# Optimization experiments

Hardware: AMD Instinct MI355X
Metric: run time of the kernel (lower is better)

## Reference

```python
import jax, jax.numpy as jnp
import numpy as np

B, T, C = 2, 2048, 2048
H, G, HS = 16, 4, 128          # n_head, n_query_groups, head_size
Q_PER_KV = H // G
SWS = 1024                      # sliding_window_size
ROPE_BASE = 10000.0


def apply_rope(x, cos, sin):
    # x: [..., T, d] with d == rope_n_elem (= head_size here); cos/sin: [T, d]
    d = x.shape[-1]
    x1, x2 = x[..., : d // 2], x[..., d // 2 :]
    rotated = jnp.concatenate((-x2, x1), axis=-1)
    return x * cos + rotated * sin


def setup_inputs() -> dict:
    key = jax.random.key(0)
    k1, k2, k3 = jax.random.split(key, 3)
    x = jax.random.normal(k1, (B, T, C), dtype=jnp.float32)
    # standard RoPE cache (litgpt-style)
    inv_freq = 1.0 / (ROPE_BASE ** (jnp.arange(0, HS, 2, dtype=jnp.float32) / HS))
    ang = jnp.outer(jnp.arange(T, dtype=jnp.float32), inv_freq)  # [T, HS/2]
    ang = jnp.concatenate((ang, ang), axis=-1)                    # [T, HS]
    cos, sin = jnp.cos(ang), jnp.sin(ang)
    W_attn = jax.random.normal(k2, ((H + 2 * G) * HS, C), dtype=jnp.float32) * 0.02
    W_proj = jax.random.normal(k3, (C, H * HS), dtype=jnp.float32) * 0.02
    return {"x": x, "cos": cos, "sin": sin, "W_attn": W_attn, "W_proj": W_proj}


def reference(x, cos, sin, W_attn, W_proj):
    # fused QKV projection: [B,T,(H+2G)*HS]
    qkv = x @ W_attn.T
    # split into groups: [B,T,G,q_per_kv+2,HS] -> [B,G,total,T,HS]
    qkv = qkv.reshape(B, T, G, Q_PER_KV + 2, HS).transpose(0, 2, 3, 1, 4)
    q = qkv[:, :, :Q_PER_KV]        # [B,G,q_per_kv,T,HS]
    k = qkv[:, :, Q_PER_KV]         # [B,G,T,HS]
    v = qkv[:, :, Q_PER_KV + 1]     # [B,G,T,HS]
    # inline RoPE (rotary_percentage=1.0 -> whole head rotated)
    q = apply_rope(q, cos, sin)
    k = apply_rope(k, cos, sin)
    # sliding-window causal mask: attend iff i-SWS < j <= i
    i = jnp.arange(T)[:, None]
    j = jnp.arange(T)[None, :]
    allowed = (j <= i) & (j > i - SWS)
    mask = jnp.where(allowed, 0.0, -jnp.inf).astype(x.dtype)  # [T,T]
    # grouped attention (k/v shared across q_per_kv heads per group, same math
    # as the torch expand+reshape)
    scale = 1.0 / np.sqrt(HS).astype(np.float32)
    scores = jnp.einsum("bgqtd,bgsd->bgqts", q, k) * scale + mask
    attn = jax.nn.softmax(scores, axis=-1)
    y = jnp.einsum("bgqts,bgsd->bgqtd", attn, v)  # [B,G,q_per_kv,T,HS]
    # [B,H,T,HS] -> [B,T,H*HS]
    y = y.reshape(B, H, T, HS).transpose(0, 2, 1, 3).reshape(B, T, H * HS)
    return y @ W_proj.T
```

## Files before the change

### kernel.cpp

```cpp
#include <hip/hip_runtime.h>
#include <hip/hip_bf16.h>
#include <cstdint>
#include <type_traits>

using bf16_t = __hip_bfloat16;
typedef __bf16 bf16x8 __attribute__((ext_vector_type(8)));
typedef float f32x4 __attribute__((ext_vector_type(4)));

typedef __attribute__((address_space(3))) uint32_t lds_u32_t;
typedef const __attribute__((address_space(1))) uint32_t glb_u32_t;

__global__ void cvt_f32_to_bf16(const float* __restrict__ in, bf16_t* __restrict__ out, int n8) {
  int stride = gridDim.x * blockDim.x;
  for (int i = blockIdx.x * blockDim.x + threadIdx.x; i < n8; i += stride) {
    const float4* p = reinterpret_cast<const float4*>(in) + (size_t)i * 2;
    float4 a = p[0];
    float4 b = p[1];
    bf16_t o[8];
    o[0] = __float2bfloat16(a.x); o[1] = __float2bfloat16(a.y);
    o[2] = __float2bfloat16(a.z); o[3] = __float2bfloat16(a.w);
    o[4] = __float2bfloat16(b.x); o[5] = __float2bfloat16(b.y);
    o[6] = __float2bfloat16(b.z); o[7] = __float2bfloat16(b.w);
    *reinterpret_cast<uint4*>(out + (size_t)i * 8) = *reinterpret_cast<const uint4*>(o);
  }
}

template <int BN, typename OutT>
__global__ __launch_bounds__(512, 2) void gemm256(const bf16_t* __restrict__ A,
                                                  const bf16_t* __restrict__ Bt,
                                                  OutT* __restrict__ C,
                                                  int M, int N, int K) {
  constexpr int JN = BN / 64;
  constexpr int JLO = (JN + 1) / 2;
  constexpr int BL = BN / 64;
  __shared__ __align__(16) bf16_t As[2 * 256 * 64];
  __shared__ __align__(16) bf16_t Bs[2 * BN * 64];
  const int tid = threadIdx.x;
  const int lane = tid & 63;
  const int w = tid >> 6;
  const int wm = w >> 2, wn = w & 3;
  const int lr = lane & 15, lc = lane >> 4;

  const int nwg = gridDim.x * gridDim.y;
  const int orig = blockIdx.y * gridDim.x + blockIdx.x;
  const int cpx = nwg >> 3;
  const int swz = (orig & 7) * cpx + (orig >> 3);
  const int bx = swz % gridDim.x, by = swz / gridDim.x;
  const int m0 = by * 256, n0 = bx * BN;

  const int srow = tid >> 3;
  const int scol = ((tid & 7) ^ (srow & 7)) * 8;
  const bf16_t* Asrc = A + (size_t)(m0 + srow) * K + scol;
  const bf16_t* Bsrc = Bt + (size_t)(n0 + srow) * K + scol;

  f32x4 acc[8][JN] = {};

  auto stageA = [&](int bufi, int kt) {
#pragma unroll
    for (int l = 0; l < 4; ++l)
      __builtin_amdgcn_global_load_lds(
          (glb_u32_t*)(Asrc + (size_t)kt * 64 + (size_t)l * 64 * K),
          (lds_u32_t*)(As + bufi * 16384 + l * 4096 + w * 512), 16, 0, 0);
  };
  auto stageB = [&](int bufi, int kt) {
#pragma unroll
    for (int l = 0; l < BL; ++l)
      __builtin_amdgcn_global_load_lds(
          (glb_u32_t*)(Bsrc + (size_t)kt * 64 + (size_t)l * 64 * K),
          (lds_u32_t*)(Bs + bufi * BN * 64 + l * 4096 + w * 512), 16, 0, 0);
  };

  const int nt = K >> 6;
  stageA(0, 0);
  stageB(0, 0);
  asm volatile("s_waitcnt vmcnt(0)" ::: "memory");
  __builtin_amdgcn_s_barrier();

  bf16x8 a[4][2], bb[JN][2];
  for (int t = 0; t < nt; ++t) {
    const int buf = t & 1;
    const char* Ab = (const char*)(As + buf * 16384);
    const char* Bb = (const char*)(Bs + buf * BN * 64);
    const bool st = (t + 1 < nt);

    auto rdA = [&](int i, int kk) {
      int R = wm * 128 + i * 16 + lr;
      return *reinterpret_cast<const bf16x8*>(
          Ab + R * 128 + ((kk * 64 + lc * 16) ^ ((R & 7) << 4)));
    };
    auto rdB = [&](int j, int kk) {
      int R = wn * (BN / 4) + j * 16 + lr;
      return *reinterpret_cast<const bf16x8*>(
          Bb + R * 128 + ((kk * 64 + lc * 16) ^ ((R & 7) << 4)));
    };

#pragma unroll
    for (int i = 0; i < 4; ++i) { a[i][0] = rdA(i, 0); a[i][1] = rdA(i, 1); }
#pragma unroll
    for (int j = 0; j < JLO; ++j) { bb[j][0] = rdB(j, 0); bb[j][1] = rdB(j, 1); }
    if (st) stageA(buf ^ 1, t + 1);
    asm volatile("" ::: "memory");
    __builtin_amdgcn_s_barrier();
    __builtin_amdgcn_s_setprio(1);
#pragma unroll
    for (int i = 0; i < 4; ++i)
#pragma unroll
      for (int j = 0; j < JLO; ++j) {
        acc[i][j] = __builtin_amdgcn_mfma_f32_16x16x32_bf16(a[i][0], bb[j][0], acc[i][j], 0, 0, 0);
        acc[i][j] = __builtin_amdgcn_mfma_f32_16x16x32_bf16(a[i][1], bb[j][1], acc[i][j], 0, 0, 0);
      }
    __builtin_amdgcn_s_setprio(0);
    asm volatile("" ::: "memory");
    __builtin_amdgcn_s_barrier();

#pragma unroll
    for (int j = JLO; j < JN; ++j) { bb[j][0] = rdB(j, 0); bb[j][1] = rdB(j, 1); }
    if (st) stageB(buf ^ 1, t + 1);
    asm volatile("" ::: "memory");
    __builtin_amdgcn_s_barrier();
    __builtin_amdgcn_s_setprio(1);
#pragma unroll
    for (int i = 0; i < 4; ++i)
#pragma unroll
      for (int j = JLO; j < JN; ++j) {
        acc[i][j] = __builtin_amdgcn_mfma_f32_16x16x32_bf16(a[i][0], bb[j][0], acc[i][j], 0, 0, 0);
        acc[i][j] = __builtin_amdgcn_mfma_f32_16x16x32_bf16(a[i][1], bb[j][1], acc[i][j], 0, 0, 0);
      }
    __builtin_amdgcn_s_setprio(0);
    asm volatile("" ::: "memory");
    __builtin_amdgcn_s_barrier();

#pragma unroll
    for (int i = 0; i < 4; ++i) { a[i][0] = rdA(i + 4, 0); a[i][1] = rdA(i + 4, 1); }
    asm volatile("" ::: "memory");
    __builtin_amdgcn_s_barrier();
    __builtin_amdgcn_s_setprio(1);
#pragma unroll
    for (int i = 0; i < 4; ++i)
#pragma unroll
      for (int j = JLO; j < JN; ++j) {
        acc[i + 4][j] = __builtin_amdgcn_mfma_f32_16x16x32_bf16(a[i][0], bb[j][0], acc[i + 4][j], 0, 0, 0);
        acc[i + 4][j] = __builtin_amdgcn_mfma_f32_16x16x32_bf16(a[i][1], bb[j][1], acc[i + 4][j], 0, 0, 0);
      }
    __builtin_amdgcn_s_setprio(0);
    asm volatile("" ::: "memory");
    __builtin_amdgcn_s_barrier();

    __builtin_amdgcn_s_setprio(1);
#pragma unroll
    for (int i = 0; i < 4; ++i)
#pragma unroll
      for (int j = 0; j < JLO; ++j) {
        acc[i + 4][j] = __builtin_amdgcn_mfma_f32_16x16x32_bf16(a[i][0], bb[j][0], acc[i + 4][j], 0, 0, 0);
        acc[i + 4][j] = __builtin_amdgcn_mfma_f32_16x16x32_bf16(a[i][1], bb[j][1], acc[i + 4][j], 0, 0, 0);
      }
    __builtin_amdgcn_s_setprio(0);

    asm volatile("s_waitcnt lgkmcnt(0)" ::: "memory");
    asm volatile("s_waitcnt vmcnt(0)" ::: "memory");
    __builtin_amdgcn_s_barrier();
  }

#pragma unroll
  for (int i = 0; i < 8; ++i)
#pragma unroll
    for (int j = 0; j < JN; ++j) {
      int row = m0 + wm * 128 + i * 16 + lc * 4;
      int col = n0 + wn * (BN / 4) + j * 16 + lr;
#pragma unroll
      for (int r = 0; r < 4; ++r) {
        float v = acc[i][j][r];
        if constexpr (std::is_same<OutT, float>::value)
          C[(size_t)(row + r) * N + col] = v;
        else
          C[(size_t)(row + r) * N + col] = __float2bfloat16(v);
      }
    }
}

__global__ __launch_bounds__(256) void rope_scatter(const bf16_t* __restrict__ qkv,
                                                    const float* __restrict__ cosp,
                                                    const float* __restrict__ sinp,
                                                    bf16_t* __restrict__ Q,
                                                    bf16_t* __restrict__ K,
                                                    bf16_t* __restrict__ V) {
  const int row = blockIdx.x;
  const int b = row >> 11, t = row & 2047;
  const bf16_t* src = qkv + (size_t)row * 3072;
  for (int n = threadIdx.x; n < 3072; n += 256) {
    int g = n / 768;
    int r = n - g * 768;
    int slot = r >> 7;
    int d = r & 127;
    if (slot == 5) {
      V[(((size_t)(b * 4 + g)) * 2048 + t) * 128 + d] = src[n];
    } else {
      float v = __bfloat162float(src[n]);
      float other = __bfloat162float(src[n ^ 64]);
      float c = cosp[t * 128 + d];
      float s = sinp[t * 128 + d];
      float rot = (d < 64) ? -other : other;
      float res = v * c + rot * s;
      if (slot < 4) {
        int h = g * 4 + slot;
        Q[(((size_t)(b * 16 + h)) * 2048 + t) * 128 + d] =
            __float2bfloat16(res * (0.08838834764831843f * 1.4426950408889634f));
      } else {
        K[(((size_t)(b * 4 + g)) * 2048 + t) * 128 + d] = __float2bfloat16(res);
      }
    }
  }
}

__global__ void transpose_v(const bf16_t* __restrict__ V, bf16_t* __restrict__ Vt) {
  __shared__ bf16_t tile[32][33];
  const int bg = blockIdx.z;
  const int t0 = blockIdx.x * 32;
  const int d0 = blockIdx.y * 32;
  const bf16_t* src = V + (size_t)bg * 2048 * 128;
  bf16_t* dst = Vt + (size_t)bg * 128 * 2048;
#pragma unroll
  for (int i = threadIdx.y; i < 32; i += 8)
    tile[i][threadIdx.x] = src[(size_t)(t0 + i) * 128 + d0 + threadIdx.x];
  __syncthreads();
#pragma unroll
  for (int i = threadIdx.y; i < 32; i += 8)
    dst[(size_t)(d0 + i) * 2048 + t0 + threadIdx.x] = tile[threadIdx.x][i];
}

#define VROW 40
__global__ __launch_bounds__(256) void attn_swa(const bf16_t* __restrict__ Q,
                                                const bf16_t* __restrict__ K,
                                                const bf16_t* __restrict__ Vt,
                                                bf16_t* __restrict__ Y) {
  __shared__ __align__(16) bf16_t Ks[2 * 32 * 128];
  __shared__ __align__(16) bf16_t Vs[2 * 128 * VROW];

  const int tid = threadIdx.x;
  const int lane = tid & 63;
  const int w = tid >> 6;
  const int lr = lane & 15, lc = lane >> 4;
  const int b = blockIdx.z, h = blockIdx.y;
  const int g = h >> 2;

  int nseg, sx0, sx1 = 0;
  if (blockIdx.x < 16) {
    nseg = 1;
    sx0 = blockIdx.x + 16;
  } else {
    nseg = 2;
    sx0 = blockIdx.x - 16;
    sx1 = 15 - sx0;
  }

  const bf16_t* Qp = Q + ((size_t)(b * 16 + h) * 2048) * 128;
  const bf16_t* Kp = K + ((size_t)(b * 4 + g) * 2048) * 128;
  const bf16_t* Vp = Vt + ((size_t)(b * 4 + g) * 128) * 2048;

  const int kmj = tid >> 4;
  const int kmc = ((tid & 15) ^ (kmj & 7)) * 8;
  const bf16_t* Ksrc = Kp + (size_t)kmj * 128 + kmc;
  const int vd = tid >> 2, vc = tid & 3;
  const bf16_t* Vsrc = Vp + (size_t)vd * 2048 + vc * 8;
  const int vdst = vd * VROW + (vc & 1) * 16 + (vc >> 1) * 4;

  auto loadK = [&](int j0, uint4& ka, uint4& kb) {
    const bf16_t* s = Ksrc + (size_t)j0 * 128;
    ka = *reinterpret_cast<const uint4*>(s);
    kb = *reinterpret_cast<const uint4*>(s + 16 * 128);
  };
  auto writeK = [&](int bufi, uint4 ka, uint4 kb) {
    *reinterpret_cast<uint4*>(Ks + bufi * 4096 + tid * 8) = ka;
    *reinterpret_cast<uint4*>(Ks + bufi * 4096 + 2048 + tid * 8) = kb;
  };
  auto loadV = [&](int j0, uint4& a, uint4& bqv) {
    a = *reinterpret_cast<const uint4*>(Vsrc + j0);
    bqv = *reinterpret_cast<const uint4*>(Vsrc + 64 * 2048 + j0);
  };
  auto writeV = [&](int bufi, uint4 a, uint4 bqv) {
    bf16_t* p = Vs + bufi * 128 * VROW + vdst;
    *reinterpret_cast<uint2*>(p) = make_uint2(a.x, a.y);
    *reinterpret_cast<uint2*>(p + 8) = make_uint2(a.z, a.w);
    bf16_t* p1 = p + 64 * VROW;
    *reinterpret_cast<uint2*>(p1) = make_uint2(bqv.x, bqv.y);
    *reinterpret_cast<uint2*>(p1 + 8) = make_uint2(bqv.z, bqv.w);
  };

  const int kxor = (lr & 7) << 4;

  for (int sidx = 0; sidx < nseg; ++sidx) {
    const int i0b = ((sidx == 0) ? sx0 : sx1) * 64;
    const int i0 = i0b + w * 16;
    const int qrow = i0 + lr;

    bf16x8 qf[4];
#pragma unroll
    for (int kc = 0; kc < 4; ++kc)
      qf[kc] = *reinterpret_cast<const bf16x8*>(&Qp[(size_t)qrow * 128 + kc * 32 + lc * 8]);

    f32x4 o[8] = {};
    float mrun = -1e30f, lrun = 0.f;

    int lo = i0b - 1023;
    if (lo < 0) lo = 0;
    const int jstart = lo & ~31;
    const int jlast = i0b + 32;

    {
      uint4 ka, kb, va, vb;
      loadK(jstart, ka, kb);
      loadV(jstart, va, vb);
      writeK(0, ka, kb);
      writeV(0, va, vb);
    }
    __syncthreads();

    int buf = 0;
    for (int j0 = jstart; j0 <= jlast; j0 += 32) {
      const int nxt = j0 + 32;
      uint4 ka, kb, va, vb;
      const bool do_stage = (nxt <= jlast);
      if (do_stage) {
        loadK(nxt, ka, kb);
        loadV(nxt, va, vb);
      }

      const bool active = (j0 <= i0 + 15) && (j0 + 31 > i0 - 1024);
      if (active) {
        const bf16_t* Kb = Ks + buf * 4096;
        const bf16_t* Vb = Vs + buf * 128 * VROW;
        f32x4 s0 = {}, s1 = {};
        __builtin_amdgcn_s_setprio(1);
#pragma unroll
        for (int kc = 0; kc < 4; ++kc) {
          int col = ((kc * 64 + lc * 16) ^ kxor) >> 1;
          bf16x8 kf0 = *reinterpret_cast<const bf16x8*>(Kb + lr * 128 + col);
          bf16x8 kf1 = *reinterpret_cast<const bf16x8*>(Kb + (16 + lr) * 128 + col);
          s0 = __builtin_amdgcn_mfma_f32_16x16x32_bf16(kf0, qf[kc], s0, 0, 0, 0);
          s1 = __builtin_amdgcn_mfma_f32_16x16x32_bf16(kf1, qf[kc], s1, 0, 0, 0);
        }
        __builtin_amdgcn_s_setprio(0);
        bf16x8 vvf[8];
#pragma unroll
        for (int f = 0; f < 8; ++f)
          vvf[f] = *reinterpret_cast<const bf16x8*>(Vb + (f * 16 + lr) * VROW + lc * 8);

        const bool full = (j0 + 31 <= i0) && (j0 >= i0 - 1008);
        if (!full) {
#pragma unroll
          for (int r = 0; r < 4; ++r) {
            int ja = j0 + lc * 4 + r;
            int jb = ja + 16;
            bool oka = (ja <= qrow) && (ja > qrow - 1024);
            bool okb = (jb <= qrow) && (jb > qrow - 1024);
            s0[r] = oka ? s0[r] : -1e30f;
            s1[r] = okb ? s1[r] : -1e30f;
          }
        }
        float rm = fmaxf(fmaxf(fmaxf(s0[0], s0[1]), fmaxf(s0[2], s0[3])),
                         fmaxf(fmaxf(s1[0], s1[1]), fmaxf(s1[2], s1[3])));

        if (!__all(rm <= mrun + 11.5f)) {
          rm = fmaxf(rm, __shfl_xor(rm, 16));
          rm = fmaxf(rm, __shfl_xor(rm, 32));
          float mnew = fmaxf(mrun, rm);
          float alpha = exp2f(mrun - mnew);
          mrun = mnew;
          lrun *= alpha;
#pragma unroll
          for (int f = 0; f < 8; ++f)
#pragma unroll
            for (int r = 0; r < 4; ++r) o[f][r] *= alpha;
        }

        float p0[4], p1[4], ps = 0.f;
#pragma unroll
        for (int r = 0; r < 4; ++r) {
          p0[r] = exp2f(s0[r] - mrun);
          p1[r] = exp2f(s1[r] - mrun);
          ps += p0[r] + p1[r];
        }
        lrun += ps;

        bf16_t pb[8];
#pragma unroll
        for (int r = 0; r < 4; ++r) {
          pb[r] = __float2bfloat16(p0[r]);
          pb[r + 4] = __float2bfloat16(p1[r]);
        }
        bf16x8 pfrag = *reinterpret_cast<bf16x8*>(pb);

        __builtin_amdgcn_s_setprio(1);
#pragma unroll
        for (int f = 0; f < 8; ++f)
          o[f] = __builtin_amdgcn_mfma_f32_16x16x32_bf16(vvf[f], pfrag, o[f], 0, 0, 0);
        __builtin_amdgcn_s_setprio(0);
      }

      if (do_stage) {
        writeK(buf ^ 1, ka, kb);
        writeV(buf ^ 1, va, vb);
      }
      __syncthreads();
      buf ^= 1;
    }

    float lt = lrun;
    lt += __shfl_xor(lt, 16);
    lt += __shfl_xor(lt, 32);
    float inv = 1.f / lt;
#pragma unroll
    for (int f = 0; f < 8; ++f) {
      bf16_t ob[4];
#pragma unroll
      for (int r = 0; r < 4; ++r) ob[r] = __float2bfloat16(o[f][r] * inv);
      *reinterpret_cast<uint2*>(
          &Y[((size_t)(b * 2048 + qrow)) * 2048 + h * 128 + f * 16 + lc * 4]) =
          *reinterpret_cast<uint2*>(ob);
    }
  }
}

extern "C" void kernel_launch(void* const* d_in, const int* in_sizes, int n_in,
                              void* d_out, int out_size, void* d_ws, size_t ws_size,
                              hipStream_t stream) {
  const float* x = (const float*)d_in[0];
  const float* cosp = (const float*)d_in[1];
  const float* sinp = (const float*)d_in[2];
  const float* Wa = (const float*)d_in[3];
  const float* Wp = (const float*)d_in[4];
  float* out = (float*)d_out;

  bf16_t* ws = (bf16_t*)d_ws;
  bf16_t* xb = ws;
  bf16_t* wab = ws + 8388608;
  bf16_t* wpb = ws + 14680064;
  bf16_t* qkv = ws + 18874368;
  bf16_t* Q = xb;
  bf16_t* Kr = wab;
  bf16_t* V = wab + 2097152;
  bf16_t* Y = qkv;
  bf16_t* Vt = qkv + 8388608;

  cvt_f32_to_bf16<<<4096, 256, 0, stream>>>(x, xb, 1048576);
  cvt_f32_to_bf16<<<3072, 256, 0, stream>>>(Wa, wab, 786432);
  cvt_f32_to_bf16<<<2048, 256, 0, stream>>>(Wp, wpb, 524288);

  gemm256<192, bf16_t><<<dim3(16, 16), 512, 0, stream>>>(xb, wab, qkv, 4096, 3072, 2048);

  rope_scatter<<<4096, 256, 0, stream>>>(qkv, cosp, sinp, Q, Kr, V);

  transpose_v<<<dim3(64, 4, 8), dim3(32, 8), 0, stream>>>(V, Vt);

  attn_swa<<<dim3(24, 16, 2), 256, 0, stream>>>(Q, Kr, Vt, Y);

  gemm256<128, float><<<dim3(16, 16), 512, 0, stream>>>(Y, wpb, out, 4096, 2048, 2048);
}
```

Measured before the change: 226.1 us.

## Restructure GEMM main loop into one MFMA phase with partial vmcnt waits

Replaces the four-phase ping-pong loop in gemm256 with a single phase per K-tile. Each tile now does one load of all A and B fragments followed by one MFMA block. Synchronisation relies on partial s_waitcnt vmcnt counts, so the next tile's async global-to-LDS loads can stay in flight across iterations instead of being drained with a full vmcnt(0) every iteration. This cuts barriers and should overlap memory with compute better. In exchange it holds all eight A fragments in registers at once, which raises register pressure under launch_bounds(512,2), and correctness depends on the hand-counted vmcnt values.

```diff
diff --git a/kernel.cpp b/kernel.cpp
--- a/kernel.cpp
+++ b/kernel.cpp
@@ -31,7 +31,6 @@
                                                   OutT* __restrict__ C,
                                                   int M, int N, int K) {
   constexpr int JN = BN / 64;
-  constexpr int JLO = (JN + 1) / 2;
   constexpr int BL = BN / 64;
   __shared__ __align__(16) bf16_t As[2 * 256 * 64];
   __shared__ __align__(16) bf16_t Bs[2 * BN * 64];
@@ -73,10 +72,8 @@
   const int nt = K >> 6;
   stageA(0, 0);
   stageB(0, 0);
-  asm volatile("s_waitcnt vmcnt(0)" ::: "memory");
-  __builtin_amdgcn_s_barrier();
-
-  bf16x8 a[4][2], bb[JN][2];
+
+  bf16x8 a[8][2], bb[JN][2];
   for (int t = 0; t < nt; ++t) {
     const int buf = t & 1;
     const char* Ab = (const char*)(As + buf * 16384);
@@ -94,71 +91,35 @@
           Bb + R * 128 + ((kk * 64 + lc * 16) ^ ((R & 7) << 4)));
     };
 
-#pragma unroll
-    for (int i = 0; i < 4; ++i) { a[i][0] = rdA(i, 0); a[i][1] = rdA(i, 1); }
-#pragma unroll
-    for (int j = 0; j < JLO; ++j) { bb[j][0] = rdB(j, 0); bb[j][1] = rdB(j, 1); }
+    if constexpr (BL == 3) {
+      asm volatile("s_waitcnt vmcnt(3)" ::: "memory");
+    } else {
+      asm volatile("s_waitcnt vmcnt(2)" ::: "memory");
+    }
+    __builtin_amdgcn_s_barrier();
+#pragma unroll
+    for (int i = 0; i < 8; ++i) { a[i][0] = rdA(i, 0); a[i][1] = rdA(i, 1); }
     if (st) stageA(buf ^ 1, t + 1);
-    asm volatile("" ::: "memory");
+
+    if (st) {
+      asm volatile("s_waitcnt vmcnt(4)" ::: "memory");
+    } else {
+      asm volatile("s_waitcnt vmcnt(0)" ::: "memory");
+    }
     __builtin_amdgcn_s_barrier();
+#pragma unroll
+    for (int j = 0; j < JN; ++j) { bb[j][0] = rdB(j, 0); bb[j][1] = rdB(j, 1); }
+    if (st) stageB(buf ^ 1, t + 1);
+
     __builtin_amdgcn_s_setprio(1);
 #pragma unroll
-    for (int i = 0; i < 4; ++i)
-#pragma unroll
-      for (int j = 0; j < JLO; ++j) {
+    for (int i = 0; i < 8; ++i)
+#pragma unroll
+      for (int j = 0; j < JN; ++j) {
         acc[i][j] = __builtin_amdgcn_mfma_f32_16x16x32_bf16(a[i][0], bb[j][0], acc[i][j], 0, 0, 0);
         acc[i][j] = __builtin_amdgcn_mfma_f32_16x16x32_bf16(a[i][1], bb[j][1], acc[i][j], 0, 0, 0);
       }
     __builtin_amdgcn_s_setprio(0);
-    asm volatile("" ::: "memory");
-    __builtin_amdgcn_s_barrier();
-
-#pragma unroll
-    for (int j = JLO; j < JN; ++j) { bb[j][0] = rdB(j, 0); bb[j][1] = rdB(j, 1); }
-    if (st) stageB(buf ^ 1, t + 1);
-    asm volatile("" ::: "memory");
-    __builtin_amdgcn_s_barrier();
-    __builtin_amdgcn_s_setprio(1);
-#pragma unroll
-    for (int i = 0; i < 4; ++i)
-#pragma unroll
-      for (int j = JLO; j < JN; ++j) {
-        acc[i][j] = __builtin_amdgcn_mfma_f32_16x16x32_bf16(a[i][0], bb[j][0], acc[i][j], 0, 0, 0);
-        acc[i][j] = __builtin_amdgcn_mfma_f32_16x16x32_bf16(a[i][1], bb[j][1], acc[i][j], 0, 0, 0);
-      }
-    __builtin_amdgcn_s_setprio(0);
-    asm volatile("" ::: "memory");
-    __builtin_amdgcn_s_barrier();
-
-#pragma unroll
-    for (int i = 0; i < 4; ++i) { a[i][0] = rdA(i + 4, 0); a[i][1] = rdA(i + 4, 1); }
-    asm volatile("" ::: "memory");
-    __builtin_amdgcn_s_barrier();
-    __builtin_amdgcn_s_setprio(1);
-#pragma unroll
-    for (int i = 0; i < 4; ++i)
-#pragma unroll
-      for (int j = JLO; j < JN; ++j) {
-        acc[i + 4][j] = __builtin_amdgcn_mfma_f32_16x16x32_bf16(a[i][0], bb[j][0], acc[i + 4][j], 0, 0, 0);
-        acc[i + 4][j] = __builtin_amdgcn_mfma_f32_16x16x32_bf16(a[i][1], bb[j][1], acc[i + 4][j], 0, 0, 0);
-      }
-    __builtin_amdgcn_s_setprio(0);
-    asm volatile("" ::: "memory");
-    __builtin_amdgcn_s_barrier();
-
-    __builtin_amdgcn_s_setprio(1);
-#pragma unroll
-    for (int i = 0; i < 4; ++i)
-#pragma unroll
-      for (int j = 0; j < JLO; ++j) {
-        acc[i + 4][j] = __builtin_amdgcn_mfma_f32_16x16x32_bf16(a[i][0], bb[j][0], acc[i + 4][j], 0, 0, 0);
-        acc[i + 4][j] = __builtin_amdgcn_mfma_f32_16x16x32_bf16(a[i][1], bb[j][1], acc[i + 4][j], 0, 0, 0);
-      }
-    __builtin_amdgcn_s_setprio(0);
-
-    asm volatile("s_waitcnt lgkmcnt(0)" ::: "memory");
-    asm volatile("s_waitcnt vmcnt(0)" ::: "memory");
-    __builtin_amdgcn_s_barrier();
   }
 
 #pragma unroll
```

After: 212.8 us. -5.9%, faster.
